# Kernel optimization log

Hardware: AMD Instinct MI355X
Metric: run time of the kernel (lower is better)

The kernel has to match this reference:

```python
import jax, jax.numpy as jnp
import numpy as np

B, T, D, U = 32, 2048, 1024, 1024

def setup_inputs() -> dict:
    key = jax.random.key(0)
    ks = jax.random.split(key, 6)
    scale = 1.0 / np.sqrt(D)
    return {
        "features": jax.random.normal(ks[0], (B, T, D), dtype=jnp.float32),
        "hidden": jax.random.normal(ks[1], (B, D), dtype=jnp.float32),
        "W1": jax.random.normal(ks[2], (D, U), dtype=jnp.float32) * scale,
        "b1": jnp.zeros((U,), dtype=jnp.float32),
        "W2": jax.random.normal(ks[3], (D, U), dtype=jnp.float32) * scale,
        "b2": jnp.zeros((U,), dtype=jnp.float32),
        "V": jax.random.normal(ks[4], (U, 1), dtype=jnp.float32) * (1.0 / np.sqrt(U)),
        "bV": jnp.zeros((1,), dtype=jnp.float32),
    }

def reference(features, hidden, W1, b1, W2, b2, V, bV):
    # features: [B,T,D], hidden: [B,D]
    proj_f = jnp.einsum('btd,du->btu', features, W1) + b1          # [B,T,U]
    proj_h = (hidden @ W2 + b2)[:, None, :]                        # [B,1,U]
    score = jnp.tanh(proj_f + proj_h)                              # [B,T,U]
    logits = jnp.einsum('btu,uo->bto', score, V) + bV              # [B,T,1]
    attention_weights = jax.nn.softmax(logits, axis=1)             # [B,T,1]
    context_vector = jnp.sum(attention_weights * features, axis=1) # [B,D]
    return context_vector, attention_weights
```

## Files before the change

### kernel.cpp

```cpp
#include <hip/hip_runtime.h>
#include <hip/hip_bf16.h>
#include <hip/hip_fp16.h>

#define B_ 32
#define T_ 2048
#define D_ 1024
#define U_ 1024
#define M_ (B_ * T_)
#define NT_ 4

typedef _Float16 f16x8 __attribute__((ext_vector_type(8)));
typedef float f32x4 __attribute__((ext_vector_type(4)));

__device__ __forceinline__ float fast_tanh(float x) {
    float xc = fminf(fmaxf(x, -10.f), 10.f);
    float e = __expf(2.f * xc);
    return 1.f - 2.f / (e + 1.f);
}

__device__ __forceinline__ void load_lds16(const void* g, void* l) {
    __builtin_amdgcn_global_load_lds(
        (const __attribute__((address_space(1))) void*)g,
        (__attribute__((address_space(3))) void*)l, 16, 0, 0);
}

__global__ void transpose_cast_kernel(const float* __restrict__ W1,
                                      _Float16* __restrict__ W1t) {
    int u = blockIdx.x * 256 + threadIdx.x;
    int d0 = blockIdx.y * 64;
    for (int j8 = 0; j8 < 8; ++j8) {
        f16x8 h;
        #pragma unroll
        for (int j = 0; j < 8; ++j)
            h[j] = (_Float16)W1[(size_t)(d0 + j8 * 8 + j) * U_ + u];
        *(f16x8*)&W1t[(size_t)u * D_ + d0 + j8 * 8] = h;
    }
}

__global__ void proj_h_partial_kernel(const float* __restrict__ hidden,
                                      const float* __restrict__ W2,
                                      float* __restrict__ pph) {
    int u = blockIdx.x * 256 + threadIdx.x;
    int c = blockIdx.y;
    __shared__ float hb[32][128];
    for (int i = threadIdx.x; i < 32 * 128; i += 256)
        hb[i >> 7][i & 127] = hidden[(i >> 7) * D_ + c * 128 + (i & 127)];
    __syncthreads();
    float acc[32] = {};
    for (int d = 0; d < 128; ++d) {
        float w = W2[(size_t)(c * 128 + d) * U_ + u];
        #pragma unroll
        for (int b = 0; b < 32; ++b) acc[b] = fmaf(hb[b][d], w, acc[b]);
    }
    #pragma unroll
    for (int b = 0; b < 32; ++b)
        pph[((size_t)c * 32 + b) * U_ + u] = acc[b];
}

__global__ void proj_h_combine_kernel(const float* __restrict__ pph,
                                      const float* __restrict__ b1,
                                      const float* __restrict__ b2,
                                      float* __restrict__ ph) {
    int u = blockIdx.x * 256 + threadIdx.x;
    float bias = b1[u] + b2[u];
    for (int b = 0; b < 32; ++b) {
        float s = bias;
        #pragma unroll
        for (int c = 0; c < 8; ++c) s += pph[((size_t)c * 32 + b) * U_ + u];
        ph[b * U_ + u] = s;
    }
}


#define ISSUE_A(koff) do { \
    const float* a0_ = pA0 + (koff); \
    const float* a1_ = pA1 + (koff); \
    araw0 = *(const f32x4*)(a0_);      araw1 = *(const f32x4*)(a0_ + 4); \
    araw2 = *(const f32x4*)(a0_ + 8);  araw3 = *(const f32x4*)(a0_ + 12); \
    araw4 = *(const f32x4*)(a1_);      araw5 = *(const f32x4*)(a1_ + 4); \
    araw6 = *(const f32x4*)(a1_ + 8);  araw7 = *(const f32x4*)(a1_ + 12); \
} while (0)

#define ISSUE_B(koffb, bufoff) do { \
    load_lds16(pB + 0 * 131072 + (koffb), smem + (bufoff) + 32768 + 0 * 8192 + tid * 16); \
    load_lds16(pB + 1 * 131072 + (koffb), smem + (bufoff) + 32768 + 1 * 8192 + tid * 16); \
    load_lds16(pB + 2 * 131072 + (koffb), smem + (bufoff) + 32768 + 2 * 8192 + tid * 16); \
    load_lds16(pB + 3 * 131072 + (koffb), smem + (bufoff) + 32768 + 3 * 8192 + tid * 16); \
} while (0)

#define WRITE_A(nbptr) do { \
    f16x8 h0_, h1_, h2_, h3_; \
    h0_[0]=(_Float16)araw0[0]; h0_[1]=(_Float16)araw0[1]; h0_[2]=(_Float16)araw0[2]; h0_[3]=(_Float16)araw0[3]; \
    h0_[4]=(_Float16)araw1[0]; h0_[5]=(_Float16)araw1[1]; h0_[6]=(_Float16)araw1[2]; h0_[7]=(_Float16)araw1[3]; \
    h1_[0]=(_Float16)araw2[0]; h1_[1]=(_Float16)araw2[1]; h1_[2]=(_Float16)araw2[2]; h1_[3]=(_Float16)araw2[3]; \
    h1_[4]=(_Float16)araw3[0]; h1_[5]=(_Float16)araw3[1]; h1_[6]=(_Float16)araw3[2]; h1_[7]=(_Float16)araw3[3]; \
    h2_[0]=(_Float16)araw4[0]; h2_[1]=(_Float16)araw4[1]; h2_[2]=(_Float16)araw4[2]; h2_[3]=(_Float16)araw4[3]; \
    h2_[4]=(_Float16)araw5[0]; h2_[5]=(_Float16)araw5[1]; h2_[6]=(_Float16)araw5[2]; h2_[7]=(_Float16)araw5[3]; \
    h3_[0]=(_Float16)araw6[0]; h3_[1]=(_Float16)araw6[1]; h3_[2]=(_Float16)araw6[2]; h3_[3]=(_Float16)araw6[3]; \
    h3_[4]=(_Float16)araw7[0]; h3_[5]=(_Float16)araw7[1]; h3_[6]=(_Float16)araw7[2]; h3_[7]=(_Float16)araw7[3]; \
    *(f16x8*)((nbptr) + aw00) = h0_; \
    *(f16x8*)((nbptr) + aw01) = h1_; \
    *(f16x8*)((nbptr) + aw10) = h2_; \
    *(f16x8*)((nbptr) + aw11) = h3_; \
} while (0)

__global__ __launch_bounds__(512, 2)
void gemm_logits_v4_kernel(const float* __restrict__ A,
                           const _Float16* __restrict__ Bt,
                           const float* __restrict__ ph,
                           const float* __restrict__ V,
                           float* __restrict__ part)
{
    __shared__ __align__(16) char smem[131072];

    int bid = blockIdx.x;
    int xcd = bid & 7, local = bid >> 3;
    int mt = xcd * 32 + (local >> 2);
    int nt = local & 3;

    int tid = threadIdx.x;
    int l = tid & 63, wid = tid >> 6;
    int wr = wid >> 2, wc = wid & 3;
    int lrow = l & 15, lksl = l >> 4;

    const float* Ag = A + (size_t)mt * 256 * D_;
    const _Float16* Bg = Bt + (size_t)nt * 256 * D_;

    const float* pA0 = Ag + (size_t)(tid >> 2) * D_ + (tid & 3) * 16;
    const float* pA1 = pA0 + (size_t)128 * D_;
    int c2 = (tid & 3) * 2;
    int r0 = tid >> 2;
    int sw = r0 & 7;
    int aw00 = r0 * 128 + ((c2 ^ sw) << 4);
    int aw01 = r0 * 128 + (((c2 | 1) ^ sw) << 4);
    int aw10 = (r0 + 128) * 128 + ((c2 ^ sw) << 4);
    int aw11 = (r0 + 128) * 128 + (((c2 | 1) ^ sw) << 4);

    int bchunk = (tid & 7) ^ ((tid >> 3) & 7);
    const char* pB = (const char*)Bg + (size_t)(tid >> 3) * 2048 + bchunk * 16;

    int rowA = (wr * 128 + lrow) * 128;
    int rowB = 32768 + (wc * 64 + lrow) * 128;
    int sw7 = lrow & 7;

    f32x4 acc[8][4] = {};
    f32x4 araw0, araw1, araw2, araw3, araw4, araw5, araw6, araw7;

    ISSUE_A(0);
    ISSUE_B(0, 0);
    WRITE_A(smem);
    __builtin_amdgcn_sched_barrier(0);
    asm volatile("s_waitcnt vmcnt(0)" ::: "memory");
    asm volatile("s_waitcnt lgkmcnt(0)" ::: "memory");
    __builtin_amdgcn_sched_barrier(0);
    __builtin_amdgcn_s_barrier();
    __builtin_amdgcn_sched_barrier(0);

    #pragma unroll 1
    for (int t = 0; t < 16; ++t) {
        const char* bb = smem + (t & 1) * 65536;
        char* nb = smem + ((t & 1) ^ 1) * 65536;
        if (t < 15) {
            ISSUE_A((t + 1) * 64);
            ISSUE_B((t + 1) * 128, ((t & 1) ^ 1) * 65536);
        }
        __builtin_amdgcn_s_setprio(1);
        #pragma unroll
        for (int kh = 0; kh < 2; ++kh) {
            int us = (((kh << 2) | lksl) ^ sw7) << 4;
            f16x8 af[8], bf[4];
            #pragma unroll
            for (int n = 0; n < 4; ++n)
                bf[n] = *(const f16x8*)(bb + rowB + n * 2048 + us);
            #pragma unroll
            for (int m = 0; m < 8; ++m)
                af[m] = *(const f16x8*)(bb + rowA + m * 2048 + us);
            #pragma unroll
            for (int m = 0; m < 8; ++m)
                #pragma unroll
                for (int n = 0; n < 4; ++n)
                    acc[m][n] = __builtin_amdgcn_mfma_f32_16x16x32_f16(
                        af[m], bf[n], acc[m][n], 0, 0, 0);
        }
        __builtin_amdgcn_s_setprio(0);
        if (t < 15) {
            WRITE_A(nb);
            __builtin_amdgcn_sched_barrier(0);
            asm volatile("s_waitcnt vmcnt(0)" ::: "memory");
            asm volatile("s_waitcnt lgkmcnt(0)" ::: "memory");
            __builtin_amdgcn_sched_barrier(0);
            __builtin_amdgcn_s_barrier();
            __builtin_amdgcn_sched_barrier(0);
        }
    }

    int bidx = mt >> 3;
    const float* phb = ph + bidx * U_;
    float Vv[4], phv[4];
    #pragma unroll
    for (int n = 0; n < 4; ++n) {
        int u = nt * 256 + wc * 64 + n * 16 + lrow;
        Vv[n] = V[u];
        phv[n] = phb[u];
    }
    float* lbuf = (float*)smem;
    #pragma unroll
    for (int m = 0; m < 8; ++m) {
        #pragma unroll
        for (int r = 0; r < 4; ++r) {
            float p = 0.f;
            #pragma unroll
            for (int n = 0; n < 4; ++n) {
                float s = fast_tanh(acc[m][n][r] + phv[n]);
                p = fmaf(s, Vv[n], p);
            }
            #pragma unroll
            for (int off = 1; off < 16; off <<= 1)
                p += __shfl_xor(p, off, 64);
            if (lrow == 0) {
                int row = wr * 128 + m * 16 + ((l >> 4) << 2) + r;
                lbuf[wc * 256 + row] = p;
            }
        }
    }
    __syncthreads();
    if (tid < 256) {
        float v = lbuf[tid] + lbuf[256 + tid] + lbuf[512 + tid] + lbuf[768 + tid];
        part[(size_t)nt * M_ + mt * 256 + tid] = v;
    }
}

__global__ void softmax_kernel(const float* __restrict__ part,
                               float* __restrict__ wout) {
    int b = blockIdx.x;
    int tid = threadIdx.x;
    __shared__ float red[8];
    float lg[8];
    #pragma unroll
    for (int j = 0; j < 8; ++j) {
        int t = tid + j * 256;
        float s = 0.f;
        #pragma unroll
        for (int p = 0; p < NT_; ++p)
            s += part[(size_t)p * M_ + b * T_ + t];
        lg[j] = s;
    }
    float mx = lg[0];
    #pragma unroll
    for (int j = 1; j < 8; ++j) mx = fmaxf(mx, lg[j]);
    #pragma unroll
    for (int off = 1; off < 64; off <<= 1) mx = fmaxf(mx, __shfl_xor(mx, off, 64));
    int wv = tid >> 6;
    if ((tid & 63) == 0) red[wv] = mx;
    __syncthreads();
    mx = fmaxf(fmaxf(red[0], red[1]), fmaxf(red[2], red[3]));
    float e[8];
    float sum = 0.f;
    #pragma unroll
    for (int j = 0; j < 8; ++j) { e[j] = __expf(lg[j] - mx); sum += e[j]; }
    #pragma unroll
    for (int off = 1; off < 64; off <<= 1) sum += __shfl_xor(sum, off, 64);
    if ((tid & 63) == 0) red[4 + wv] = sum;
    __syncthreads();
    sum = red[4] + red[5] + red[6] + red[7];
    float inv = 1.f / sum;
    #pragma unroll
    for (int j = 0; j < 8; ++j)
        wout[b * T_ + tid + j * 256] = e[j] * inv;
}

#define TCH 128
__global__ void context_partial_kernel(const float* __restrict__ feats,
                                       const float* __restrict__ w,
                                       float* __restrict__ cpart) {
    int b = blockIdx.x, tc = blockIdx.y, tid = threadIdx.x;
    f32x4 acc = {0.f, 0.f, 0.f, 0.f};
    const float* f = feats + ((size_t)b * T_ + tc * TCH) * D_ + tid * 4;
    const float* wp = w + b * T_ + tc * TCH;
    for (int t = 0; t < TCH; ++t) {
        float wt = wp[t];
        f32x4 fv = *(const f32x4*)(f + (size_t)t * D_);
        acc[0] = fmaf(wt, fv[0], acc[0]);
        acc[1] = fmaf(wt, fv[1], acc[1]);
        acc[2] = fmaf(wt, fv[2], acc[2]);
        acc[3] = fmaf(wt, fv[3], acc[3]);
    }
    *(f32x4*)&cpart[((size_t)tc * B_ + b) * D_ + tid * 4] = acc;
}

__global__ void context_reduce_kernel(const float* __restrict__ cpart,
                                      float* __restrict__ out) {
    int i = blockIdx.x * 256 + threadIdx.x;
    float s = 0.f;
    #pragma unroll
    for (int tc = 0; tc < 16; ++tc)
        s += cpart[(size_t)tc * (B_ * D_) + i];
    out[i] = s;
}

extern "C" void kernel_launch(void* const* d_in, const int* in_sizes, int n_in,
                              void* d_out, int out_size, void* d_ws, size_t ws_size,
                              hipStream_t stream) {
    const float* features = (const float*)d_in[0];
    const float* hidden   = (const float*)d_in[1];
    const float* W1       = (const float*)d_in[2];
    const float* b1       = (const float*)d_in[3];
    const float* W2       = (const float*)d_in[4];
    const float* b2       = (const float*)d_in[5];
    const float* V        = (const float*)d_in[6];

    float* ctx_out = (float*)d_out;
    float* w_out   = ctx_out + B_ * D_;

    char* ws = (char*)d_ws;
    _Float16* W1t = (_Float16*)ws;
    float* ph     = (float*)(ws + (size_t)(2 << 20));
    float* pph    = (float*)(ws + (size_t)(3 << 20));
    float* part   = (float*)(ws + (size_t)(4 << 20));
    float* cpart  = (float*)(ws + (size_t)(6 << 20));

    transpose_cast_kernel<<<dim3(4, 16), 256, 0, stream>>>(W1, W1t);
    proj_h_partial_kernel<<<dim3(4, 8), 256, 0, stream>>>(hidden, W2, pph);
    proj_h_combine_kernel<<<4, 256, 0, stream>>>(pph, b1, b2, ph);

    gemm_logits_v4_kernel<<<(M_ / 256) * (U_ / 256), 512, 0, stream>>>(
        features, W1t, ph, V, part);

    softmax_kernel<<<B_, 256, 0, stream>>>(part, w_out);
    context_partial_kernel<<<dim3(B_, 16), 256, 0, stream>>>(features, w_out, cpart);
    context_reduce_kernel<<<(B_ * D_) / 256, 256, 0, stream>>>(cpart, ctx_out);
}
```

Measured before the change: 297.1 us.

## Restructure GEMM main loop into four barrier-synchronized MFMA phases with split LDS buffers

```diff
diff --git a/kernel.cpp b/kernel.cpp
--- a/kernel.cpp
+++ b/kernel.cpp
@@ -72,6 +72,11 @@
 }
 
 
+#define SB0 __builtin_amdgcn_sched_barrier(0);
+#define BAR __builtin_amdgcn_s_barrier();
+#define LGKM0 asm volatile("s_waitcnt lgkmcnt(0)" ::: "memory");
+#define VM0 asm volatile("s_waitcnt vmcnt(0)" ::: "memory");
+
 #define ISSUE_A(koff) do { \
     const float* a0_ = pA0 + (koff); \
     const float* a1_ = pA1 + (koff); \
@@ -82,10 +87,10 @@
 } while (0)
 
 #define ISSUE_B(koffb, bufoff) do { \
-    load_lds16(pB + 0 * 131072 + (koffb), smem + (bufoff) + 32768 + 0 * 8192 + tid * 16); \
-    load_lds16(pB + 1 * 131072 + (koffb), smem + (bufoff) + 32768 + 1 * 8192 + tid * 16); \
-    load_lds16(pB + 2 * 131072 + (koffb), smem + (bufoff) + 32768 + 2 * 8192 + tid * 16); \
-    load_lds16(pB + 3 * 131072 + (koffb), smem + (bufoff) + 32768 + 3 * 8192 + tid * 16); \
+    load_lds16(pB + 0 * 131072 + (koffb), smem + (bufoff) + 0 * 8192 + tid * 16); \
+    load_lds16(pB + 1 * 131072 + (koffb), smem + (bufoff) + 1 * 8192 + tid * 16); \
+    load_lds16(pB + 2 * 131072 + (koffb), smem + (bufoff) + 2 * 8192 + tid * 16); \
+    load_lds16(pB + 3 * 131072 + (koffb), smem + (bufoff) + 3 * 8192 + tid * 16); \
 } while (0)
 
 #define WRITE_A(nbptr) do { \
@@ -104,8 +109,40 @@
     *(f16x8*)((nbptr) + aw11) = h3_; \
 } while (0)
 
-__global__ __launch_bounds__(512, 2)
-void gemm_logits_v4_kernel(const float* __restrict__ A,
+#define MFMA16(mh) do { \
+    _Pragma("unroll") \
+    for (int m_ = 0; m_ < 4; ++m_) { \
+        _Pragma("unroll") \
+        for (int n_ = 0; n_ < 4; ++n_) \
+            acc[(mh) * 4 + m_][n_] = __builtin_amdgcn_mfma_f32_16x16x32_f16( \
+                af[m_], bf[n_], acc[(mh) * 4 + m_][n_], 0, 0, 0); \
+    } \
+} while (0)
+
+#define READ_AF(kh, mh) do { \
+    int us_ = ((((kh) << 2) | lksl) ^ sw7) << 4; \
+    _Pragma("unroll") \
+    for (int m_ = 0; m_ < 4; ++m_) \
+        af[m_] = *(const f16x8*)(cbA + rowA + ((mh) * 4 + m_) * 2048 + us_); \
+} while (0)
+
+#define READ_BF(kh) do { \
+    int us_ = ((((kh) << 2) | lksl) ^ sw7) << 4; \
+    _Pragma("unroll") \
+    for (int n_ = 0; n_ < 4; ++n_) \
+        bf[n_] = *(const f16x8*)(cbB + rowB + n_ * 2048 + us_); \
+} while (0)
+
+#define PHASE_SYNC(mh) do { \
+    SB0 BAR LGKM0 SB0 \
+    __builtin_amdgcn_s_setprio(1); \
+    MFMA16(mh); \
+    __builtin_amdgcn_s_setprio(0); \
+    SB0 BAR SB0 \
+} while (0)
+
+__global__ __launch_bounds__(512, 1)
+void gemm_logits_v5_kernel(const float* __restrict__ A,
                            const _Float16* __restrict__ Bt,
                            const float* __restrict__ ph,
                            const float* __restrict__ V,
@@ -122,6 +159,7 @@
     int l = tid & 63, wid = tid >> 6;
     int wr = wid >> 2, wc = wid & 3;
     int lrow = l & 15, lksl = l >> 4;
+    int sw7 = lrow & 7;
 
     const float* Ag = A + (size_t)mt * 256 * D_;
     const _Float16* Bg = Bt + (size_t)nt * 256 * D_;
@@ -140,58 +178,48 @@
     const char* pB = (const char*)Bg + (size_t)(tid >> 3) * 2048 + bchunk * 16;
 
     int rowA = (wr * 128 + lrow) * 128;
-    int rowB = 32768 + (wc * 64 + lrow) * 128;
-    int sw7 = lrow & 7;
+    int rowB = (wc * 64 + lrow) * 128;
 
     f32x4 acc[8][4] = {};
     f32x4 araw0, araw1, araw2, araw3, araw4, araw5, araw6, araw7;
-
+    f16x8 af[4], bf[4];
+
+    ISSUE_B(0, 65536);
     ISSUE_A(0);
-    ISSUE_B(0, 0);
+    SB0 VM0 SB0
     WRITE_A(smem);
-    __builtin_amdgcn_sched_barrier(0);
-    asm volatile("s_waitcnt vmcnt(0)" ::: "memory");
-    asm volatile("s_waitcnt lgkmcnt(0)" ::: "memory");
-    __builtin_amdgcn_sched_barrier(0);
-    __builtin_amdgcn_s_barrier();
-    __builtin_amdgcn_sched_barrier(0);
+    LGKM0 SB0
+    BAR SB0
 
     #pragma unroll 1
     for (int t = 0; t < 16; ++t) {
-        const char* bb = smem + (t & 1) * 65536;
-        char* nb = smem + ((t & 1) ^ 1) * 65536;
-        if (t < 15) {
+        const char* cbA = smem + (t & 1) * 32768;
+        const char* cbB = smem + 65536 + (t & 1) * 32768;
+        char* nbA = smem + ((t & 1) ^ 1) * 32768;
+        int nbB = 65536 + (((t & 1) ^ 1)) * 32768;
+        bool pf = (t < 15);
+
+        READ_BF(0);
+        READ_AF(0, 0);
+        if (pf) {
+            ISSUE_B((t + 1) * 128, nbB);
             ISSUE_A((t + 1) * 64);
-            ISSUE_B((t + 1) * 128, ((t & 1) ^ 1) * 65536);
         }
-        __builtin_amdgcn_s_setprio(1);
-        #pragma unroll
-        for (int kh = 0; kh < 2; ++kh) {
-            int us = (((kh << 2) | lksl) ^ sw7) << 4;
-            f16x8 af[8], bf[4];
-            #pragma unroll
-            for (int n = 0; n < 4; ++n)
-                bf[n] = *(const f16x8*)(bb + rowB + n * 2048 + us);
-            #pragma unroll
-            for (int m = 0; m < 8; ++m)
-                af[m] = *(const f16x8*)(bb + rowA + m * 2048 + us);
-            #pragma unroll
-            for (int m = 0; m < 8; ++m)
-                #pragma unroll
-                for (int n = 0; n < 4; ++n)
-                    acc[m][n] = __builtin_amdgcn_mfma_f32_16x16x32_f16(
-                        af[m], bf[n], acc[m][n], 0, 0, 0);
+        PHASE_SYNC(0);
+
+        READ_AF(0, 1);
+        PHASE_SYNC(1);
+
+        READ_BF(1);
+        READ_AF(1, 0);
+        PHASE_SYNC(0);
+
+        READ_AF(1, 1);
+        if (pf) {
+            SB0 VM0 SB0
+            WRITE_A(nbA);
         }
-        __builtin_amdgcn_s_setprio(0);
-        if (t < 15) {
-            WRITE_A(nb);
-            __builtin_amdgcn_sched_barrier(0);
-            asm volatile("s_waitcnt vmcnt(0)" ::: "memory");
-            asm volatile("s_waitcnt lgkmcnt(0)" ::: "memory");
-            __builtin_amdgcn_sched_barrier(0);
-            __builtin_amdgcn_s_barrier();
-            __builtin_amdgcn_sched_barrier(0);
-        }
+        PHASE_SYNC(1);
     }
 
     int bidx = mt >> 3;
@@ -323,7 +351,7 @@
     proj_h_partial_kernel<<<dim3(4, 8), 256, 0, stream>>>(hidden, W2, pph);
     proj_h_combine_kernel<<<4, 256, 0, stream>>>(pph, b1, b2, ph);
 
-    gemm_logits_v4_kernel<<<(M_ / 256) * (U_ / 256), 512, 0, stream>>>(
+    gemm_logits_v5_kernel<<<(M_ / 256) * (U_ / 256), 512, 0, stream>>>(
         features, W1t, ph, V, part);
 
     softmax_kernel<<<B_, 256, 0, stream>>>(part, w_out);
```

Result: slower. 326.6 us (+9.9%).
